# Performance work log

Hardware: AMD Instinct MI355X
Metric: run time of the kernel (lower is better)

## Reference

```python
import jax, jax.numpy as jnp
import numpy as np

NS = 33  # segments per image: id 0 = background, 1..32 = objects (fixed max-object count)
EPS_GN = 1e-5


def conv2d(x, w, b, pad):
    y = jax.lax.conv_general_dilated(x, w, window_strides=(1, 1),
                                     padding=[(pad, pad), (pad, pad)],
                                     dimension_numbers=('NCHW', 'OIHW', 'NCHW'))
    return y + b[None, :, None, None]


def group_norm(x, gamma, beta, groups):
    B, C, H, W = x.shape
    xg = x.reshape(B, groups, C // groups, H, W)
    mu = xg.mean((2, 3, 4), keepdims=True)
    var = xg.var((2, 3, 4), keepdims=True)
    xn = ((xg - mu) / jnp.sqrt(var + EPS_GN)).reshape(B, C, H, W)
    return xn * gamma[None, :, None, None] + beta[None, :, None, None]


def setup_inputs() -> dict:
    key = jax.random.key(0)
    ks = jax.random.split(key, 10)
    B, Cf, H, W = 4, 512, 128, 128
    std = 0.01
    inp = {
        'x': jax.random.normal(ks[0], (B, Cf, H, W), jnp.float32),
        'masks': jax.random.randint(ks[1], (B, H, W), 0, NS).astype(jnp.int32),
        # coord_conv: Conv2d(2, 64, 1)
        'w_coord': jax.random.normal(ks[2], (64, 2, 1, 1), jnp.float32) * std,
        'b_coord': jnp.zeros((64,), jnp.float32),
        # encoder convs + groupnorms
        'w1': jax.random.normal(ks[3], (256, Cf + 64, 3, 3), jnp.float32) * std,
        'b1': jnp.zeros((256,), jnp.float32),
        'g1': jnp.ones((256,), jnp.float32), 'bt1': jnp.zeros((256,), jnp.float32),
        'w2': jax.random.normal(ks[4], (128, 256, 3, 3), jnp.float32) * std,
        'b2': jnp.zeros((128,), jnp.float32),
        'g2': jnp.ones((128,), jnp.float32), 'bt2': jnp.zeros((128,), jnp.float32),
        'w3': jax.random.normal(ks[5], (64, 128, 3, 3), jnp.float32) * std,
        'b3': jnp.zeros((64,), jnp.float32),
        'g3': jnp.ones((64,), jnp.float32), 'bt3': jnp.zeros((64,), jnp.float32),
        # heads (1x1 convs on pooled [64] vectors == tiny matmuls)
        'w_box': jax.random.normal(ks[6], (7, 64, 1, 1), jnp.float32) * std,
        'b_box': jnp.zeros((7,), jnp.float32),
        'w_conf': jax.random.normal(ks[7], (1, 64, 1, 1), jnp.float32) * std,
        'b_conf': jnp.zeros((1,), jnp.float32),
    }
    return inp


def reference(x, masks, w_coord, b_coord, w1, b1, g1, bt1, w2, b2, g2, bt2,
              w3, b3, g3, bt3, w_box, b_box, w_conf, b_conf):
    B, _, H, W = x.shape
    # coordinate grid: channels are [grid_x, grid_y]
    gy, gx = jnp.meshgrid(jnp.arange(H), jnp.arange(W), indexing='ij')
    grid = jnp.stack([gx, gy], axis=0).astype(x.dtype)            # [2,H,W]
    grid = jnp.broadcast_to(grid[None], (B, 2, H, W))
    grid_feats = jax.nn.relu(conv2d(grid, w_coord, b_coord, 0))   # [B,64,H,W]

    h = jnp.concatenate([x, grid_feats], axis=1)                  # [B,576,H,W]
    h = jax.nn.relu(group_norm(conv2d(h, w1, b1, 1), g1, bt1, 8))
    h = jax.nn.relu(group_norm(conv2d(h, w2, b2, 1), g2, bt2, 4))
    h = jax.nn.relu(group_norm(conv2d(h, w3, b3, 1), g3, bt3, 4))  # [B,64,H,W]

    # per-(image, object-id) masked mean pooling via segment_sum
    C = h.shape[1]
    flat = h.transpose(0, 2, 3, 1).reshape(-1, C)                 # [B*H*W, 64]
    seg = (jnp.arange(B, dtype=jnp.int32)[:, None] * NS
           + masks.reshape(B, -1)).reshape(-1)                    # [B*H*W]
    sums = jax.ops.segment_sum(flat, seg, num_segments=B * NS).reshape(B, NS, C)
    counts = jax.ops.segment_sum(jnp.ones_like(seg, jnp.float32), seg,
                                 num_segments=B * NS).reshape(B, NS, 1)
    # drop background segment 0; safe divide matches the <1e-4 skip (empty slots -> 0 pooled)
    pooled = sums[:, 1:] / jnp.maximum(counts[:, 1:], 1e-4)       # [B,32,64]

    boxes = jnp.einsum('boc,kc->bok', pooled, w_box.reshape(7, C)) + b_box   # [B,32,7]
    scores = jnp.einsum('boc,c->bo', pooled, w_conf.reshape(C)) + b_conf[0]  # [B,32]
    return boxes, scores
```

## Files before the change

kernel.cpp:

```cpp
#include <hip/hip_runtime.h>

typedef unsigned short u16;
typedef unsigned int u32;
typedef __bf16 bf16x8 __attribute__((ext_vector_type(8)));
typedef float f32x4 __attribute__((ext_vector_type(4)));

__device__ __forceinline__ u16 f2bf(float f) {
  u32 u = __float_as_uint(f);
  u += 0x7fffu + ((u >> 16) & 1u);
  return (u16)(u >> 16);
}
__device__ __forceinline__ float bf2f(u16 h) {
  return __uint_as_float(((u32)h) << 16);
}

#define GLD_LDS16(g, l)                                                        \
  __builtin_amdgcn_global_load_lds(                                            \
      (__attribute__((address_space(1))) void*)(g),                            \
      (__attribute__((address_space(3))) void*)(l), 16, 0, 0)

__global__ __launch_bounds__(256) void init_k(float* smallb, u16* in1, u16* in2,
                                              u16* in3) {
  int bid = blockIdx.x;
  if (bid < 35) {
    int i = bid * 256 + threadIdx.x;
    if (i < 8708) smallb[i] = 0.f;
    return;
  }
  u16* buf;
  int C, sub;
  if (bid < 51)      { buf = in1; C = 576; sub = bid - 35; }
  else if (bid < 67) { buf = in2; C = 256; sub = bid - 51; }
  else               { buf = in3; C = 128; sub = bid - 67; }
  int b = sub >> 2, s = sub & 3;
  int npx = (s < 2) ? 130 : 128;
  u32* base = (u32*)(buf + (size_t)b * 130 * 130 * C);
  int C2 = C >> 1;
  int total = npx * C2;
  for (int i = threadIdx.x; i < total; i += 256) {
    int p = i / C2, r = i - p * C2;
    int y, x;
    if (s == 0)      { y = 0;     x = p; }
    else if (s == 1) { y = 129;   x = p; }
    else if (s == 2) { y = p + 1; x = 0; }
    else             { y = p + 1; x = 129; }
    base[(y * 130 + x) * C2 + r] = 0u;
  }
}

__global__ __launch_bounds__(256) void repack_all(const float* __restrict__ w1,
                                                  u16* __restrict__ wp1,
                                                  const float* __restrict__ w2,
                                                  u16* __restrict__ wp2,
                                                  const float* __restrict__ w3,
                                                  u16* __restrict__ wp3) {
  int bid = blockIdx.x;
  const float* src;
  u16* dst;
  int CIN, COUT, total, base;
  if (bid < 5184)      { src = w1; dst = wp1; CIN = 576; COUT = 256; total = 1327104; base = bid; }
  else if (bid < 6336) { src = w2; dst = wp2; CIN = 256; COUT = 128; total = 294912;  base = bid - 5184; }
  else                 { src = w3; dst = wp3; CIN = 128; COUT = 64;  total = 73728;   base = bid - 6336; }
  int idx = base * 256 + threadIdx.x;
  if (idx >= total) return;
  int kc = idx & 31;
  int n = (idx >> 5) % COUT;
  int q = idx / (32 * COUT);
  int dydx = q % 9, cb = q / 9;
  dst[idx] = f2bf(src[((size_t)n * CIN + cb * 32 + kc) * 9 + dydx]);
}

__global__ __launch_bounds__(256) void transpose_x(const float* __restrict__ x,
                                                   const float* __restrict__ wcd,
                                                   const float* __restrict__ bcd,
                                                   u16* __restrict__ in1) {
  const int bid = blockIdx.x;
  const int b = bid >> 8, h = (bid >> 1) & 127, half = bid & 1;
  const int w0 = half * 64;
  const int t = threadIdx.x;
  __shared__ u16 tile[128 * 65];
  __shared__ float swc[128], sbc[64];
  if (t < 128) swc[t] = wcd[t];
  else if (t < 192) sbc[t - 128] = bcd[t - 128];
  const int w = t & 63;
  const int cg = t >> 6;
  const float* xb = x + (((size_t)b * 512) * 128 + h) * 128 + w0 + w;
  u16* ob = in1 + ((size_t)(b * 130 + h + 1) * 130 + (w0 + 1)) * 576;
#pragma unroll 1
  for (int cc = 0; cc < 4; ++cc) {
    const int c0 = cc * 128;
#pragma unroll
    for (int j = 0; j < 32; ++j) {
      int cl = j * 4 + cg;
      tile[cl * 65 + w] = f2bf(xb[(size_t)(c0 + cl) * 16384]);
    }
    __syncthreads();
#pragma unroll
    for (int k = 0; k < 4; ++k) {
      int idx = k * 256 + t;
      int ww = idx >> 4, c8 = (idx & 15) * 8;
      union { uint4 u; u16 s[8]; } o;
#pragma unroll
      for (int i = 0; i < 8; ++i) o.s[i] = tile[(c8 + i) * 65 + ww];
      *(uint4*)(ob + (size_t)ww * 576 + c0 + c8) = o.u;
    }
    __syncthreads();
  }
  const int px = t >> 2, cq = (t & 3) * 16;
  const float fw = (float)(w0 + px), fh = (float)h;
  u16* gp = ob + (size_t)px * 576 + 512 + cq;
#pragma unroll
  for (int j = 0; j < 2; ++j) {
    union { uint4 u; u16 s[8]; } o;
#pragma unroll
    for (int i = 0; i < 8; ++i) {
      int c = cq + j * 8 + i;
      float v = swc[2 * c] * fw + swc[2 * c + 1] * fh + sbc[c];
      o.s[i] = f2bf(fmaxf(v, 0.f));
    }
    *(uint4*)(gp + j * 8) = o.u;
  }
}

template <int CIN, int COUT, int BN>
__global__ __launch_bounds__(256) void conv3x3_k(const u16* __restrict__ in,
                                                 const u16* __restrict__ wp,
                                                 const float* __restrict__ bias,
                                                 u16* __restrict__ out, int Hp,
                                                 int Wp, int opy, int opx,
                                                 float* __restrict__ stats,
                                                 int gsLog2, int nG) {
  constexpr int CB = CIN / 32;
  constexpr int WN = BN / 2;
  constexpr int NT = WN / 16;
  constexpr int ROWCH = 520;
  constexpr int NCH = 3 * ROWCH;
  static_assert(BN == 128 || BN == 64, "");
  __shared__ u16 As3[3 * 130 * 32];
  __shared__ float redS[8], redQ[8];

  const int t = threadIdx.x;
  const int L = gridDim.x;
  const int work = (blockIdx.x & 7) * (L >> 3) + (blockIdx.x >> 3);
  const int xt = work >> 9;
  const int rem = work & 511;
  const int b = rem >> 7, h = rem & 127;
  const int n0 = xt * BN;

  const int lane = t & 63, wv = t >> 6;
  const int wm = wv & 1, wn = wv >> 1;
  const int ln = lane & 15, lq = lane >> 4;

  if (t < 8) { redS[t] = 0.f; redQ[t] = 0.f; }

  f32x4 acc[4][NT];
  const f32x4 zero = {0.f, 0.f, 0.f, 0.f};
#pragma unroll
  for (int i = 0; i < 4; ++i)
#pragma unroll
    for (int j = 0; j < NT; ++j) acc[i][j] = zero;

  const u16* inb = in + ((size_t)b * 130 + h) * 130 * CIN;

#pragma unroll 1
  for (int cb = 0; cb < CB; ++cb) {
    __syncthreads();
    const u16* slab = inb + cb * 32;
#pragma unroll
    for (int it = 0; it < 7; ++it) {
      int c = it * 256 + t;
      if (c < NCH) {
        int r = (c >= 2 * ROWCH) ? 2 : (c >= ROWCH ? 1 : 0);
        int wch = c - r * ROWCH;
        int pxi = wch >> 2, q = wch & 3;
        int qs = q ^ ((pxi >> 1) & 3);
        GLD_LDS16(slab + (r * 130 + pxi) * CIN + qs * 8, &As3[c * 8]);
      }
    }
    __syncthreads();
    const u16* wcb =
        wp + ((size_t)(cb * 9) * COUT + n0 + wn * WN + ln) * 32 + lq * 8;
#pragma unroll
    for (int dydx = 0; dydx < 9; ++dydx) {
      const int dy = dydx / 3, dx = dydx % 3;
      bf16x8 fa[4], fb[NT];
#pragma unroll
      for (int j = 0; j < NT; ++j)
        fb[j] = *(const bf16x8*)(wcb + (size_t)dydx * COUT * 32 + j * 512);
#pragma unroll
      for (int i = 0; i < 4; ++i) {
        int pxl = dx + wm * 64 + i * 16 + ln;
        int qs = lq ^ ((pxl >> 1) & 3);
        fa[i] = *(const bf16x8*)&As3[((dy * 130 + pxl) << 5) + qs * 8];
      }
#pragma unroll
      for (int i = 0; i < 4; ++i)
#pragma unroll
        for (int j = 0; j < NT; ++j)
          acc[i][j] = __builtin_amdgcn_mfma_f32_16x16x32_bf16(fa[i], fb[j],
                                                              acc[i][j], 0, 0, 0);
    }
  }

#pragma unroll
  for (int j = 0; j < NT; ++j) {
    const int n = n0 + wn * WN + j * 16 + ln;
    const float bv = bias[n];
    float sj = 0.f, qj = 0.f;
#pragma unroll
    for (int i = 0; i < 4; ++i) {
#pragma unroll
      for (int r = 0; r < 4; ++r) {
        const int w = wm * 64 + i * 16 + lq * 4 + r;
        u16 st = f2bf(acc[i][j][r] + bv);
        out[((size_t)(b * Hp + h + opy) * Wp + (w + opx)) * COUT + n] = st;
        float vq = bf2f(st);
        sj += vq;
        qj += vq * vq;
      }
    }
    sj += __shfl_xor(sj, 16, 64);
    sj += __shfl_xor(sj, 32, 64);
    qj += __shfl_xor(qj, 16, 64);
    qj += __shfl_xor(qj, 32, 64);
    if (lq == 0) {
      int gl = (wn * WN + j * 16 + ln) >> gsLog2;
      atomicAdd(&redS[gl], sj);
      atomicAdd(&redQ[gl], qj);
    }
  }
  __syncthreads();
  if (t < (BN >> gsLog2)) {
    int g = (n0 >> gsLog2) + t;
    atomicAdd(&stats[b * nG + g], redS[t]);
    atomicAdd(&stats[4 * nG + b * nG + g], redQ[t]);
  }
}

__global__ __launch_bounds__(256) void gn_norm(u16* __restrict__ buf,
                                               const float* __restrict__ stats,
                                               const float* __restrict__ gamma,
                                               const float* __restrict__ beta,
                                               int C, int gsLog2, int nG,
                                               float invCnt, int Hp, int Wp,
                                               int py, int px) {
  const int t = threadIdx.x;
  const int mt = blockIdx.x;
  const int b = mt >> 7, h = mt & 127;
  __shared__ float la[256], lb[256];
  for (int i = t; i < C; i += 256) {
    int g = i >> gsLog2;
    float mean = stats[b * nG + g] * invCnt;
    float m2 = stats[4 * nG + b * nG + g] * invCnt;
    float rstd = rsqrtf(m2 - mean * mean + 1e-5f);
    float a = gamma[i] * rstd;
    la[i] = a;
    lb[i] = beta[i] - mean * a;
  }
  __syncthreads();
  u16* row = buf + ((size_t)(b * Hp + h + py) * Wp + px) * C;
  const int n8 = 128 * C / 8;
  for (int v = t; v < n8; v += 256) {
    uint4 d = *(uint4*)(row + v * 8);
    int c0 = (v * 8) & (C - 1);
    u16* pp = (u16*)&d;
    union { uint4 u; u16 s[8]; } o;
#pragma unroll
    for (int i = 0; i < 8; ++i) {
      float xx = bf2f(pp[i]);
      float y = la[c0 + i] * xx + lb[c0 + i];
      o.s[i] = f2bf(fmaxf(y, 0.f));
    }
    *(uint4*)(row + v * 8) = o.u;
  }
}

__global__ __launch_bounds__(256) void pool_k(const u16* __restrict__ h3,
                                              const int* __restrict__ masks,
                                              const float* __restrict__ stats,
                                              const float* __restrict__ gamma,
                                              const float* __restrict__ beta,
                                              float* __restrict__ gsum,
                                              float* __restrict__ gcnt) {
  const int t = threadIdx.x;
  const int b = blockIdx.x >> 6, chunk = blockIdx.x & 63;
  __shared__ float ls[33 * 64];
  __shared__ float lc[33];
  for (int i = t; i < 33 * 64; i += 256) ls[i] = 0.f;
  if (t < 33) lc[t] = 0.f;
  const int c = t & 63;
  const int g = c >> 4;
  const float invCnt = 1.f / (16384.f * 16.f);
  float mean = stats[b * 4 + g] * invCnt;
  float m2 = stats[16 + b * 4 + g] * invCnt;
  float rstd = rsqrtf(m2 - mean * mean + 1e-5f);
  const float a = gamma[c] * rstd;
  const float cc = beta[c] - mean * a;
  __syncthreads();
  const int p0 = chunk * 256;
  for (int i = 0; i < 64; ++i) {
    int p = p0 + i * 4 + (t >> 6);
    int id = masks[b * 16384 + p];
    float v = bf2f(h3[((size_t)b * 16384 + p) * 64 + c]);
    v = fmaxf(a * v + cc, 0.f);
    atomicAdd(&ls[id * 64 + c], v);
    if (c == 0) atomicAdd(&lc[id], 1.f);
  }
  __syncthreads();
  for (int i = t; i < 33 * 64; i += 256) atomicAdd(&gsum[b * 2112 + i], ls[i]);
  if (t < 33) atomicAdd(&gcnt[b * 33 + t], lc[t]);
}

__global__ __launch_bounds__(256) void heads_k(const float* __restrict__ gsum,
                                               const float* __restrict__ gcnt,
                                               const float* __restrict__ wbox,
                                               const float* __restrict__ bbox,
                                               const float* __restrict__ wconf,
                                               const float* __restrict__ bconf,
                                               float* __restrict__ out) {
  int idx = blockIdx.x * 256 + threadIdx.x;
  if (idx >= 1024) return;
  if (idx < 896) {
    int b = idx / 224, r = idx % 224;
    int o = r / 7, k = r % 7;
    float inv = 1.f / fmaxf(gcnt[b * 33 + o + 1], 1e-4f);
    const float* ps = gsum + (b * 33 + o + 1) * 64;
    float s = 0.f;
    for (int c = 0; c < 64; ++c) s += ps[c] * wbox[k * 64 + c];
    out[idx] = s * inv + bbox[k];
  } else {
    int i = idx - 896;
    int b = i >> 5, o = i & 31;
    float inv = 1.f / fmaxf(gcnt[b * 33 + o + 1], 1e-4f);
    const float* ps = gsum + (b * 33 + o + 1) * 64;
    float s = 0.f;
    for (int c = 0; c < 64; ++c) s += ps[c] * wconf[c];
    out[896 + i] = s * inv + bconf[0];
  }
}

extern "C" void kernel_launch(void* const* d_in, const int* in_sizes, int n_in,
                              void* d_out, int out_size, void* d_ws,
                              size_t ws_size, hipStream_t stream) {
  (void)in_sizes; (void)n_in; (void)out_size; (void)ws_size;
  const float* x       = (const float*)d_in[0];
  const int*   masks   = (const int*)d_in[1];
  const float* w_coord = (const float*)d_in[2];
  const float* b_coord = (const float*)d_in[3];
  const float* w1  = (const float*)d_in[4];
  const float* b1  = (const float*)d_in[5];
  const float* g1  = (const float*)d_in[6];
  const float* bt1 = (const float*)d_in[7];
  const float* w2  = (const float*)d_in[8];
  const float* b2  = (const float*)d_in[9];
  const float* g2  = (const float*)d_in[10];
  const float* bt2 = (const float*)d_in[11];
  const float* w3  = (const float*)d_in[12];
  const float* b3  = (const float*)d_in[13];
  const float* g3  = (const float*)d_in[14];
  const float* bt3 = (const float*)d_in[15];
  const float* wbox  = (const float*)d_in[16];
  const float* bbox  = (const float*)d_in[17];
  const float* wconf = (const float*)d_in[18];
  const float* bconf = (const float*)d_in[19];
  float* out = (float*)d_out;

  char* ws = (char*)d_ws;
  size_t off = 0;
  auto take = [&](size_t bytes) {
    size_t o = off;
    off += (bytes + 255) & ~(size_t)255;
    return o;
  };
  u16* in1 = (u16*)(ws + take((size_t)4 * 130 * 130 * 576 * 2));
  u16* in2 = (u16*)(ws + take((size_t)4 * 130 * 130 * 256 * 2));
  u16* in3 = (u16*)(ws + take((size_t)4 * 130 * 130 * 128 * 2));
  u16* wp1 = (u16*)(ws + take((size_t)9 * 576 * 256 * 2));
  u16* wp2 = (u16*)(ws + take((size_t)9 * 256 * 128 * 2));
  u16* wp3 = (u16*)(ws + take((size_t)9 * 128 * 64 * 2));
  float* smallb = (float*)(ws + take(8708 * 4));
  u16* h3 = in1;

  float* s1   = smallb;
  float* s2   = smallb + 64;
  float* s3   = smallb + 96;
  float* psum = smallb + 128;
  float* pcnt = smallb + 8576;

  init_k<<<dim3(83), 256, 0, stream>>>(smallb, in1, in2, in3);

  repack_all<<<dim3(6624), 256, 0, stream>>>(w1, wp1, w2, wp2, w3, wp3);

  transpose_x<<<dim3(1024), 256, 0, stream>>>(x, w_coord, b_coord, in1);

  conv3x3_k<576, 256, 128><<<dim3(1024), 256, 0, stream>>>(in1, wp1, b1, in2, 130, 130, 1, 1, s1, 5, 8);
  gn_norm<<<dim3(512), 256, 0, stream>>>(in2, s1, g1, bt1, 256, 5, 8, 1.f / (16384.f * 32.f), 130, 130, 1, 1);

  conv3x3_k<256, 128, 128><<<dim3(512), 256, 0, stream>>>(in2, wp2, b2, in3, 130, 130, 1, 1, s2, 5, 4);
  gn_norm<<<dim3(512), 256, 0, stream>>>(in3, s2, g2, bt2, 128, 5, 4, 1.f / (16384.f * 32.f), 130, 130, 1, 1);

  conv3x3_k<128, 64, 64><<<dim3(512), 256, 0, stream>>>(in3, wp3, b3, h3, 128, 128, 0, 0, s3, 4, 4);

  pool_k<<<dim3(256), 256, 0, stream>>>(h3, masks, s3, g3, bt3, psum, pcnt);
  heads_k<<<dim3(4), 256, 0, stream>>>(psum, pcnt, wbox, bbox, wconf, bconf, out);
}
```

Measured before the change: 595.9 us.

## Double-buffer conv3x3 LDS input slabs and prefetch next weight fragments

```diff
diff --git a/kernel.cpp b/kernel.cpp
--- a/kernel.cpp
+++ b/kernel.cpp
@@ -135,8 +135,9 @@
   constexpr int NT = WN / 16;
   constexpr int ROWCH = 520;
   constexpr int NCH = 3 * ROWCH;
+  constexpr int BUFE = 3 * 130 * 32;
   static_assert(BN == 128 || BN == 64, "");
-  __shared__ u16 As3[3 * 130 * 32];
+  __shared__ u16 As3[2 * BUFE];
   __shared__ float redS[8], redQ[8];
 
   const int t = threadIdx.x;
@@ -162,36 +163,56 @@
 
   const u16* inb = in + ((size_t)b * 130 + h) * 130 * CIN;
 
+  int sc[7], srp[7], sqs[7];
+#pragma unroll
+  for (int it = 0; it < 7; ++it) {
+    int c = it * 256 + t;
+    sc[it] = (c < NCH) ? c : -1;
+    int r = (c >= 2 * ROWCH) ? 2 : (c >= ROWCH ? 1 : 0);
+    int wch = c - r * ROWCH;
+    int pxi = wch >> 2, q = wch & 3;
+    srp[it] = (r * 130 + pxi) * CIN + (q ^ ((pxi >> 1) & 3)) * 8;
+    sqs[it] = c * 8;
+  }
+
+  auto stage = [&](int cb, int sel) {
+    const u16* slab = inb + cb * 32;
+    u16* dst = &As3[sel * BUFE];
+#pragma unroll
+    for (int it = 0; it < 7; ++it)
+      if (sc[it] >= 0) GLD_LDS16(slab + srp[it], dst + sqs[it]);
+  };
+
+  stage(0, 0);
+
+  const u16* wbase0 = wp + ((size_t)n0 + wn * WN + ln) * 32 + lq * 8;
+
 #pragma unroll 1
   for (int cb = 0; cb < CB; ++cb) {
     __syncthreads();
-    const u16* slab = inb + cb * 32;
-#pragma unroll
-    for (int it = 0; it < 7; ++it) {
-      int c = it * 256 + t;
-      if (c < NCH) {
-        int r = (c >= 2 * ROWCH) ? 2 : (c >= ROWCH ? 1 : 0);
-        int wch = c - r * ROWCH;
-        int pxi = wch >> 2, q = wch & 3;
-        int qs = q ^ ((pxi >> 1) & 3);
-        GLD_LDS16(slab + (r * 130 + pxi) * CIN + qs * 8, &As3[c * 8]);
-      }
-    }
-    __syncthreads();
-    const u16* wcb =
-        wp + ((size_t)(cb * 9) * COUT + n0 + wn * WN + ln) * 32 + lq * 8;
+    const int cur = cb & 1;
+    if (cb + 1 < CB) stage(cb + 1, 1 - cur);
+    const u16* wcb = wbase0 + (size_t)(cb * 9) * COUT * 32;
+    const u16* As = &As3[cur * BUFE];
+
+    bf16x8 fb[NT], fbn[NT];
+#pragma unroll
+    for (int j = 0; j < NT; ++j)
+      fb[j] = *(const bf16x8*)(wcb + j * 512);
 #pragma unroll
     for (int dydx = 0; dydx < 9; ++dydx) {
       const int dy = dydx / 3, dx = dydx % 3;
-      bf16x8 fa[4], fb[NT];
-#pragma unroll
-      for (int j = 0; j < NT; ++j)
-        fb[j] = *(const bf16x8*)(wcb + (size_t)dydx * COUT * 32 + j * 512);
+      if (dydx < 8) {
+#pragma unroll
+        for (int j = 0; j < NT; ++j)
+          fbn[j] = *(const bf16x8*)(wcb + (size_t)(dydx + 1) * COUT * 32 + j * 512);
+      }
+      bf16x8 fa[4];
 #pragma unroll
       for (int i = 0; i < 4; ++i) {
         int pxl = dx + wm * 64 + i * 16 + ln;
         int qs = lq ^ ((pxl >> 1) & 3);
-        fa[i] = *(const bf16x8*)&As3[((dy * 130 + pxl) << 5) + qs * 8];
+        fa[i] = *(const bf16x8*)&As[((dy * 130 + pxl) << 5) + qs * 8];
       }
 #pragma unroll
       for (int i = 0; i < 4; ++i)
@@ -199,6 +220,8 @@
         for (int j = 0; j < NT; ++j)
           acc[i][j] = __builtin_amdgcn_mfma_f32_16x16x32_bf16(fa[i], fb[j],
                                                               acc[i][j], 0, 0, 0);
+#pragma unroll
+      for (int j = 0; j < NT; ++j) fb[j] = fbn[j];
     }
   }
 
```

New measurement: 596.5 us. No clear change (+0.1%).
